# Optimization experiments

Hardware: AMD Instinct MI355X
Metric: run time of the kernel (lower is better)

## Reference

```python
import jax, jax.numpy as jnp
import numpy as np

RADIUS = 0.2
NSAMPLE = 32
EPS = 1e-5  # BatchNorm2d default eps


def _bn_relu(x, g, b):
    # BatchNorm2d in training mode: per-channel stats over (B, S, nsample), biased var.
    m = x.mean(axis=(0, 1, 2))
    v = jnp.mean((x - m) ** 2, axis=(0, 1, 2))
    return jax.nn.relu((x - m) * jax.lax.rsqrt(v + EPS) * g + b)


def setup_inputs() -> dict:
    key = jax.random.key(0)
    ks = jax.random.split(key, 8)
    B, N, S = 8, 8192, 2048
    xyz = jax.random.uniform(ks[0], (B, 3, N), dtype=jnp.float32)          # unit cube
    points = jax.random.normal(ks[1], (B, 3, N), dtype=jnp.float32)
    fps_idx = jax.random.randint(ks[2], (B, S), 0, N, dtype=jnp.int32)
    W1 = jax.random.normal(ks[3], (64, 6), dtype=jnp.float32) * 0.1
    W2 = jax.random.normal(ks[4], (64, 64), dtype=jnp.float32) * 0.1
    W3 = jax.random.normal(ks[5], (128, 64), dtype=jnp.float32) * 0.1
    return dict(
        xyz=xyz, points=points, fps_idx=fps_idx,
        W1=W1, g1=jnp.ones((64,)), b1=jnp.zeros((64,)),
        W2=W2, g2=jnp.ones((64,)), b2=jnp.zeros((64,)),
        W3=W3, g3=jnp.ones((128,)), b3=jnp.zeros((128,)),
    )


def reference(xyz, points, fps_idx, W1, g1, b1, W2, g2, b2, W3, g3, b3):
    B, _, N = xyz.shape
    xyz_t = jnp.transpose(xyz, (0, 2, 1))            # [B,N,3]
    pts_t = jnp.transpose(points, (0, 2, 1))         # [B,N,D]
    # gather_operation: sampled centers
    new_xyz_t = jnp.take_along_axis(xyz_t, fps_idx[:, :, None], axis=1)  # [B,S,3]
    # ball query: first NSAMPLE points within radius; pad with first hit
    d2 = jnp.sum((new_xyz_t[:, :, None, :] - xyz_t[:, None, :, :]) ** 2, axis=-1)  # [B,S,N]
    keys = jnp.where(d2 <= RADIUS * RADIUS, jnp.arange(N, dtype=jnp.int32), N)
    neg_top, _ = jax.lax.top_k(-keys, NSAMPLE)       # smallest keys first
    idx = -neg_top                                   # [B,S,NSAMPLE]
    idx = jnp.where(idx < N, idx, idx[:, :, 0:1])    # pad empty slots with first hit (self always in-radius)
    bidx = jnp.arange(B)[:, None, None]
    grouped_xyz = xyz_t[bidx, idx]                   # [B,S,ns,3]
    rel = grouped_xyz - new_xyz_t[:, :, None, :]     # center-relative coords
    grouped_pts = pts_t[bidx, idx]                   # [B,S,ns,D]
    feat = jnp.concatenate([rel, grouped_pts], axis=-1)  # [B,S,ns,3+D]
    for W, g, b in ((W1, g1, b1), (W2, g2, b2), (W3, g3, b3)):
        feat = _bn_relu(jnp.einsum('bsnc,oc->bsno', feat, W), g, b)
    new_points = jnp.max(feat, axis=2)               # max over neighbors -> [B,S,C]
    return jnp.transpose(new_xyz_t, (0, 2, 1)), jnp.transpose(new_points, (0, 2, 1))
```

## Files before the change

kernel.cpp:

```cpp
#include <hip/hip_runtime.h>
#include <hip/hip_bf16.h>

#define BB_ 8
#define NN_ 8192
#define SS_ 2048
#define NS 32
#define C1 64
#define C2 64
#define C3 128
#define RAD2 0.04f
#define BN_EPS 1e-5f
#define M_TOT (BB_*SS_*NS)
#define INV_M (1.0f/524288.0f)
#define YSTR 34

typedef __attribute__((ext_vector_type(8))) short bf16x8;
typedef __attribute__((ext_vector_type(4))) float f32x4;

#define FBF_OFF 0
#define WPK_OFF 2097152
#define ST_OFF  2104320
#define GMM_OFF 2104832

__device__ inline unsigned pkbf(float a, float b) {
    __hip_bfloat162 h = __float22bfloat162_rn(make_float2(a, b));
    unsigned r; __builtin_memcpy(&r, &h, 4); return r;
}
__device__ inline bf16x8 asfrag(uint4 v) { bf16x8 r; __builtin_memcpy(&r, &v, 16); return r; }
__device__ inline float bflo(unsigned u) { unsigned x = u << 16; float f; __builtin_memcpy(&f, &x, 4); return f; }
__device__ inline float bfhi(unsigned u) { unsigned x = u & 0xffff0000u; float f; __builtin_memcpy(&f, &x, 4); return f; }

__device__ inline void fin1_ch(const float* __restrict__ st, const float* __restrict__ W1,
                               const float* __restrict__ g, const float* __restrict__ bb,
                               int o, float* __restrict__ al, float* __restrict__ cl) {
    float w[6];
    #pragma unroll
    for (int i = 0; i < 6; ++i) w[i] = W1[o * 6 + i];
    float ms = 0.f;
    #pragma unroll
    for (int i = 0; i < 6; ++i) ms = fmaf(w[i], st[i], ms);
    float m = ms * INV_M;
    float e2 = 0.f;
    #pragma unroll
    for (int ci = 0; ci < 6; ++ci)
        #pragma unroll
        for (int d = 0; d < 6; ++d) {
            int lo = ci < d ? ci : d, hi = ci < d ? d : ci;
            int idx = 6 + lo * 6 - lo * (lo + 1) / 2 + hi;
            e2 = fmaf(w[ci] * w[d], st[idx], e2);
        }
    float var = e2 * INV_M - m * m;
    float ai = g[o] * (1.0f / sqrtf(var + BN_EPS));
    al[o] = ai;
    cl[o] = bb[o] - m * ai;
}

__device__ inline void fin_ch(const float* __restrict__ sum, const float* __restrict__ sq,
                              const float* __restrict__ g, const float* __restrict__ bb,
                              int o, float* __restrict__ al, float* __restrict__ cl) {
    float m = sum[o] * INV_M;
    float var = sq[o] * INV_M - m * m;
    float ai = g[o] * (1.0f / sqrtf(var + BN_EPS));
    al[o] = ai;
    cl[o] = bb[o] - m * ai;
}

__global__ void k_front(const float* __restrict__ xyz, const float* __restrict__ pts,
                        const int* __restrict__ fps, uint4* __restrict__ fbf,
                        const float* __restrict__ W1, const float* __restrict__ W2,
                        const float* __restrict__ W3, uint4* __restrict__ wf,
                        float* __restrict__ st) {
    __shared__ int lidx[4][NS];
    int tid = threadIdx.x;
    if (blockIdx.x >= 4096) {
        int bb = blockIdx.x - 4096;
        if (bb == 7) { st[tid] = 0.f; st[tid + 256] = 0.f; return; }
        int t = bb * 256 + tid;
        int l = t & 63, p = l & 15, qd = l >> 4;
        float v[8];
        if (t < 256) {
            int mt = t >> 6;
            #pragma unroll
            for (int j = 0; j < 8; ++j)
                v[j] = (qd == 0 && j < 6) ? W1[(mt * 16 + p) * 6 + j] : 0.f;
        } else if (t < 768) {
            int fr = (t - 256) >> 6;
            int mt = fr >> 1, kf = fr & 1;
            #pragma unroll
            for (int j = 0; j < 8; ++j)
                v[j] = W2[(16 * mt + p) * 64 + kf * 32 + qd * 8 + j];
        } else {
            int fr = (t - 768) >> 6;
            int nt = fr >> 1, kf = fr & 1;
            #pragma unroll
            for (int j = 0; j < 8; ++j)
                v[j] = W3[(nt * 16 + p) * 64 + kf * 32 + qd * 8 + j];
        }
        uint4 o;
        o.x = pkbf(v[0], v[1]); o.y = pkbf(v[2], v[3]);
        o.z = pkbf(v[4], v[5]); o.w = pkbf(v[6], v[7]);
        wf[t] = o;
        return;
    }
    int wave = (blockIdx.x * blockDim.x + tid) >> 6;
    int lane = tid & 63;
    int wslot = tid >> 6;
    int b = wave / SS_;
    const float* xb = xyz + (size_t)b * 3 * NN_;
    const float* pb = pts + (size_t)b * 3 * NN_;
    int ci = fps[wave];
    float cx = xb[ci], cy = xb[NN_ + ci], cz = xb[2 * NN_ + ci];

    float px = xb[lane], py = xb[NN_ + lane], pz = xb[2 * NN_ + lane];
    int found = 0;
    int first_i = -1;
    for (int base = 0; base < NN_; base += 64) {
        float xv = px, yv = py, zv = pz;
        int nb = (base + 64 < NN_) ? base + 64 : 0;
        px = xb[nb + lane]; py = xb[NN_ + nb + lane]; pz = xb[2 * NN_ + nb + lane];
        float dx = xv - cx, dy = yv - cy, dz = zv - cz;
        float d2 = __fadd_rn(__fadd_rn(__fmul_rn(dx, dx), __fmul_rn(dy, dy)), __fmul_rn(dz, dz));
        bool inr = d2 <= RAD2;
        unsigned long long mask = __ballot(inr);
        if (first_i < 0 && mask) first_i = base + __builtin_ctzll(mask);
        if (inr) {
            int pos = found + __popcll(mask & ((1ull << lane) - 1ull));
            if (pos < NS) lidx[wslot][pos] = base + lane;
        }
        found += __popcll(mask);
        if (found >= NS) break;
    }
    if (found > NS) found = NS;
    if (lane < NS) {
        int j = (lane < found) ? lidx[wslot][lane] : first_i;
        uint4 o;
        o.x = pkbf(xb[j] - cx,           xb[NN_ + j] - cy);
        o.y = pkbf(xb[2 * NN_ + j] - cz, pb[j]);
        o.z = pkbf(pb[NN_ + j],          pb[2 * NN_ + j]);
        o.w = 0u;
        fbf[(size_t)wave * NS + lane] = o;
    }
}

__global__ void k_p1(const uint4* __restrict__ fbf, float* __restrict__ st) {
    __shared__ float sacc[27];
    int tid = threadIdx.x;
    if (tid < 27) sacc[tid] = 0.f;
    __syncthreads();
    int gt = blockIdx.x * 256 + tid;
    float vals[27];
    #pragma unroll
    for (int i = 0; i < 27; ++i) vals[i] = 0.f;
    #pragma unroll 1
    for (int it = 0; it < M_TOT / 262144; ++it) {
        uint4 w = fbf[it * 262144 + gt];
        float f[6] = { bflo(w.x), bfhi(w.x), bflo(w.y), bfhi(w.y), bflo(w.z), bfhi(w.z) };
        #pragma unroll
        for (int c = 0; c < 6; ++c) vals[c] += f[c];
        int q = 6;
        #pragma unroll
        for (int c = 0; c < 6; ++c)
            #pragma unroll
            for (int d = c; d < 6; ++d) { vals[q] = fmaf(f[c], f[d], vals[q]); ++q; }
    }
    int lane = tid & 63;
    #pragma unroll
    for (int i = 0; i < 27; ++i) {
        float v = vals[i];
        #pragma unroll
        for (int d = 32; d; d >>= 1) v += __shfl_xor(v, d);
        if (lane == 0) atomicAdd(&sacc[i], v);
    }
    __syncthreads();
    if (tid < 27) atomicAdd(&st[tid], sacc[tid]);
}

__global__ __launch_bounds__(256, 4) void k_p2(
        const uint4* __restrict__ fbf, const uint4* __restrict__ wpk,
        float* __restrict__ st,
        const float* __restrict__ W1, const float* __restrict__ g1, const float* __restrict__ b1) {
    __shared__ unsigned yls[4][64 * YSTR];
    __shared__ float bs[C2], bq[C2];
    __shared__ float a1ls[C1], c1ls[C1];
    int tid = threadIdx.x, wslot = tid >> 6, lane = tid & 63;
    int p = lane & 15, qd = lane >> 4;
    int tile0 = blockIdx.x * 8 + wslot;
    uint4 bv[4];
    #pragma unroll
    for (int nt = 0; nt < 4; ++nt) {
        uint4 v = make_uint4(0u, 0u, 0u, 0u);
        if (qd == 0) v = fbf[tile0 * 64 + nt * 16 + p];
        bv[nt] = v;
    }
    bf16x8 w1r[4];
    #pragma unroll
    for (int mt = 0; mt < 4; ++mt) w1r[mt] = asfrag(wpk[mt * 64 + lane]);
    if (tid < C2) { bs[tid] = 0.f; bq[tid] = 0.f; fin1_ch(st, W1, g1, b1, tid, a1ls, c1ls); }
    __syncthreads();
    const uint4* w2f = wpk + 256;
    unsigned* my = yls[wslot];
    float s2[4][4], q2[4][4];
    #pragma unroll
    for (int i = 0; i < 4; ++i)
        #pragma unroll
        for (int r = 0; r < 4; ++r) { s2[i][r] = 0.f; q2[i][r] = 0.f; }

    #pragma unroll
    for (int t = 0; t < 2; ++t) {
        uint4 nbv[4];
        if (t == 0) {
            #pragma unroll
            for (int nt = 0; nt < 4; ++nt) {
                uint4 v = make_uint4(0u, 0u, 0u, 0u);
                if (qd == 0) v = fbf[(tile0 + 4) * 64 + nt * 16 + p];
                nbv[nt] = v;
            }
        }
        bf16x8 B1[4];
        #pragma unroll
        for (int nt = 0; nt < 4; ++nt) B1[nt] = asfrag(bv[nt]);
        #pragma unroll
        for (int mt = 0; mt < 4; ++mt) {
            bf16x8 A = w1r[mt];
            float4 av = *(const float4*)(a1ls + mt * 16 + qd * 4);
            float4 cv = *(const float4*)(c1ls + mt * 16 + qd * 4);
            #pragma unroll
            for (int nt = 0; nt < 4; ++nt) {
                f32x4 acc = {0.f, 0.f, 0.f, 0.f};
                acc = __builtin_amdgcn_mfma_f32_16x16x32_bf16(A, B1[nt], acc, 0, 0, 0);
                float y0 = fmaxf(fmaf(av.x, acc[0], cv.x), 0.f);
                float y1 = fmaxf(fmaf(av.y, acc[1], cv.y), 0.f);
                float y2 = fmaxf(fmaf(av.z, acc[2], cv.z), 0.f);
                float y3 = fmaxf(fmaf(av.w, acc[3], cv.w), 0.f);
                int a = (nt * 16 + p) * YSTR + mt * 8 + qd * 2;
                *(uint2*)&my[a] = make_uint2(pkbf(y0, y1), pkbf(y2, y3));
            }
        }
        asm volatile("" ::: "memory");
        bf16x8 B2[4][2];
        #pragma unroll
        for (int nt = 0; nt < 4; ++nt)
            #pragma unroll
            for (int kf = 0; kf < 2; ++kf)
                B2[nt][kf] = asfrag(*(const uint4*)&my[(nt * 16 + p) * YSTR + kf * 16 + qd * 4]);
        asm volatile("" ::: "memory");
        #pragma unroll
        for (int mt = 0; mt < 4; ++mt) {
            f32x4 acc[4];
            #pragma unroll
            for (int nt = 0; nt < 4; ++nt) acc[nt] = (f32x4){0.f, 0.f, 0.f, 0.f};
            #pragma unroll
            for (int kf = 0; kf < 2; ++kf) {
                bf16x8 W = asfrag(w2f[(mt * 2 + kf) * 64 + lane]);
                #pragma unroll
                for (int nt = 0; nt < 4; ++nt)
                    acc[nt] = __builtin_amdgcn_mfma_f32_16x16x32_bf16(W, B2[nt][kf], acc[nt], 0, 0, 0);
            }
            #pragma unroll
            for (int r = 0; r < 4; ++r) {
                float u0 = acc[0][r], u1 = acc[1][r], u2 = acc[2][r], u3 = acc[3][r];
                s2[mt][r] += (u0 + u1) + (u2 + u3);
                q2[mt][r] = fmaf(u0, u0, fmaf(u1, u1, fmaf(u2, u2, fmaf(u3, u3, q2[mt][r]))));
            }
        }
        if (t == 0) {
            #pragma unroll
            for (int nt = 0; nt < 4; ++nt) bv[nt] = nbv[nt];
        }
        asm volatile("" ::: "memory");
    }
    #pragma unroll
    for (int mt = 0; mt < 4; ++mt)
        #pragma unroll
        for (int r = 0; r < 4; ++r) {
            float s = s2[mt][r], q = q2[mt][r];
            #pragma unroll
            for (int off = 1; off <= 8; off <<= 1) { s += __shfl_xor(s, off); q += __shfl_xor(q, off); }
            if (p == 0) {
                atomicAdd(&bs[mt * 16 + qd * 4 + r], s);
                atomicAdd(&bq[mt * 16 + qd * 4 + r], q);
            }
        }
    __syncthreads();
    if (tid < C2) { atomicAdd(&st[64 + tid], bs[tid]); atomicAdd(&st[128 + tid], bq[tid]); }
}

__global__ __launch_bounds__(256, 4) void k_p3_fused(
        const uint4* __restrict__ fbf, const uint4* __restrict__ wpk,
        float* __restrict__ st,
        const float* __restrict__ W1, const float* __restrict__ g1, const float* __restrict__ b1,
        const float* __restrict__ g2, const float* __restrict__ b2,
        const float* __restrict__ g3, float* __restrict__ gmm) {
    __shared__ unsigned yls[4][64 * YSTR];
    __shared__ float bs[C3], bq[C3];
    __shared__ float a1ls[C1], c1ls[C1], a2ls[C2], c2ls[C2];
    int tid = threadIdx.x, wslot = tid >> 6, lane = tid & 63;
    int p = lane & 15, qd = lane >> 4;
    int tile0 = blockIdx.x * 4 + wslot;
    unsigned posm = 0;
    #pragma unroll
    for (int i = 0; i < 8; ++i) posm |= (g3[i * 16 + p] >= 0.f) ? (1u << i) : 0u;
    if (tid < 128) bs[tid] = 0.f; else bq[tid - 128] = 0.f;
    if (tid < 64) fin1_ch(st, W1, g1, b1, tid, a1ls, c1ls);
    else if (tid < 128) fin_ch(st + 64, st + 128, g2, b2, tid - 64, a2ls, c2ls);
    __syncthreads();
    const uint4* w1f = wpk;
    const uint4* w2f = wpk + 256;
    const uint4* w3f = wpk + 768;
    unsigned* my = yls[wslot];

    #pragma unroll 1
    for (int it = 0; it < 2; ++it) {
        int tile = tile0 + it * 4096;
        uint4 bv[4];
        #pragma unroll
        for (int nt = 0; nt < 4; ++nt) {
            uint4 v = make_uint4(0u, 0u, 0u, 0u);
            if (qd == 0) v = fbf[tile * 64 + nt * 16 + p];
            bv[nt] = v;
        }
        #pragma unroll
        for (int mt = 0; mt < 4; ++mt) {
            bf16x8 Aw = asfrag(w1f[mt * 64 + lane]);
            float4 av = *(const float4*)(a1ls + mt * 16 + qd * 4);
            float4 cv = *(const float4*)(c1ls + mt * 16 + qd * 4);
            #pragma unroll
            for (int nt = 0; nt < 4; ++nt) {
                f32x4 acc = {0.f, 0.f, 0.f, 0.f};
                acc = __builtin_amdgcn_mfma_f32_16x16x32_bf16(Aw, asfrag(bv[nt]), acc, 0, 0, 0);
                float y0 = fmaxf(fmaf(av.x, acc[0], cv.x), 0.f);
                float y1 = fmaxf(fmaf(av.y, acc[1], cv.y), 0.f);
                float y2 = fmaxf(fmaf(av.z, acc[2], cv.z), 0.f);
                float y3 = fmaxf(fmaf(av.w, acc[3], cv.w), 0.f);
                int a = (nt * 16 + p) * YSTR + mt * 8 + qd * 2;
                *(uint2*)&my[a] = make_uint2(pkbf(y0, y1), pkbf(y2, y3));
            }
        }
        asm volatile("" ::: "memory");
        bf16x8 B2[4][2];
        #pragma unroll
        for (int nt = 0; nt < 4; ++nt)
            #pragma unroll
            for (int kf = 0; kf < 2; ++kf)
                B2[nt][kf] = asfrag(*(const uint4*)&my[(nt * 16 + p) * YSTR + kf * 16 + qd * 4]);
        asm volatile("" ::: "memory");
        #pragma unroll
        for (int mt = 0; mt < 4; ++mt) {
            f32x4 acc[4];
            #pragma unroll
            for (int nt = 0; nt < 4; ++nt) acc[nt] = (f32x4){0.f, 0.f, 0.f, 0.f};
            #pragma unroll
            for (int kf = 0; kf < 2; ++kf) {
                bf16x8 W = asfrag(w2f[(mt * 2 + kf) * 64 + lane]);
                #pragma unroll
                for (int nt = 0; nt < 4; ++nt)
                    acc[nt] = __builtin_amdgcn_mfma_f32_16x16x32_bf16(W, B2[nt][kf], acc[nt], 0, 0, 0);
            }
            float4 av = *(const float4*)(a2ls + mt * 16 + qd * 4);
            float4 cv = *(const float4*)(c2ls + mt * 16 + qd * 4);
            #pragma unroll
            for (int nt = 0; nt < 4; ++nt) {
                float y0 = fmaxf(fmaf(av.x, acc[nt][0], cv.x), 0.f);
                float y1 = fmaxf(fmaf(av.y, acc[nt][1], cv.y), 0.f);
                float y2 = fmaxf(fmaf(av.z, acc[nt][2], cv.z), 0.f);
                float y3 = fmaxf(fmaf(av.w, acc[nt][3], cv.w), 0.f);
                int a = (nt * 16 + p) * YSTR + mt * 8 + qd * 2;
                *(uint2*)&my[a] = make_uint2(pkbf(y0, y1), pkbf(y2, y3));
            }
        }
        asm volatile("" ::: "memory");
        bf16x8 A3[4][2];
        #pragma unroll
        for (int mt = 0; mt < 4; ++mt) {
            A3[mt][0] = asfrag(*(const uint4*)&my[(mt * 16 + p) * YSTR + qd * 4]);
            A3[mt][1] = asfrag(*(const uint4*)&my[(mt * 16 + p) * YSTR + 16 + qd * 4]);
        }
        asm volatile("" ::: "memory");
        uint4 wva = w3f[lane];
        uint4 wvb = w3f[64 + lane];
        #pragma unroll 1
        for (int nt = 0; nt < 8; ++nt) {
            int nn = (nt < 7) ? nt + 1 : 7;
            uint4 nwa = w3f[(nn * 2 + 0) * 64 + lane];
            uint4 nwb = w3f[(nn * 2 + 1) * 64 + lane];
            bf16x8 Wa = asfrag(wva), Wb = asfrag(wvb);
            f32x4 acc[4];
            #pragma unroll
            for (int mt = 0; mt < 4; ++mt) {
                acc[mt] = __builtin_amdgcn_mfma_f32_16x16x32_bf16(A3[mt][0], Wa,
                            (f32x4){0.f, 0.f, 0.f, 0.f}, 0, 0, 0);
                acc[mt] = __builtin_amdgcn_mfma_f32_16x16x32_bf16(A3[mt][1], Wb, acc[mt], 0, 0, 0);
            }
            bool pn = (posm >> nt) & 1;
            float s = 0.f, q = 0.f, va = 0.f, vb = 0.f;
            #pragma unroll
            for (int mt = 0; mt < 4; ++mt) {
                float v0 = acc[mt][0], v1 = acc[mt][1], v2 = acc[mt][2], v3 = acc[mt][3];
                s += (v0 + v1) + (v2 + v3);
                q = fmaf(v0, v0, fmaf(v1, v1, fmaf(v2, v2, fmaf(v3, v3, q))));
                float mx = fmaxf(fmaxf(v0, v1), fmaxf(v2, v3));
                float mn = fminf(fminf(v0, v1), fminf(v2, v3));
                float vv = pn ? mx : -mn;
                if (mt == 0) va = vv;
                else if (mt == 1) va = fmaxf(va, vv);
                else if (mt == 2) vb = vv;
                else vb = fmaxf(vb, vv);
            }
            s += __shfl_xor(s, 16); s += __shfl_xor(s, 32);
            q += __shfl_xor(q, 16); q += __shfl_xor(q, 32);
            va = fmaxf(va, __shfl_xor(va, 16)); va = fmaxf(va, __shfl_xor(va, 32));
            vb = fmaxf(vb, __shfl_xor(vb, 16)); vb = fmaxf(vb, __shfl_xor(vb, 32));
            if (lane < 16) {
                gmm[(size_t)(tile * 2 + 0) * C3 + nt * 16 + lane] = va;
                gmm[(size_t)(tile * 2 + 1) * C3 + nt * 16 + lane] = vb;
                atomicAdd(&bs[nt * 16 + lane], s);
                atomicAdd(&bq[nt * 16 + lane], q);
            }
            wva = nwa; wvb = nwb;
        }
    }
    __syncthreads();
    if (tid < C3) { atomicAdd(&st[192 + tid], bs[tid]); atomicAdd(&st[320 + tid], bq[tid]); }
}

__global__ void k_outx(const float* __restrict__ gmm, const float* __restrict__ st,
                       const float* __restrict__ g3, const float* __restrict__ b3,
                       const float* __restrict__ xyz, const int* __restrict__ fps,
                       float* __restrict__ out) {
    __shared__ float T[C3][17];
    __shared__ float a3ls[C3], c3ls[C3];
    int blk = blockIdx.x, tid = threadIdx.x;
    if (blk < 1024) {
        if (tid < C3) fin_ch(st + 192, st + 320, g3, b3, tid, a3ls, c3ls);
        __syncthreads();
        int b = blk >> 7, s0 = (blk & 127) << 4;
        #pragma unroll
        for (int i = 0; i < 8; ++i) {
            int idx = i * 256 + tid;
            int sl = idx >> 7, o = idx & 127;
            float m = gmm[((size_t)(b * SS_ + s0 + sl)) * C3 + o];
            float a = a3ls[o];
            float v = (a >= 0.f) ? m : -m;
            T[o][sl] = fmaxf(fmaf(a, v, c3ls[o]), 0.f);
        }
        __syncthreads();
        int o = tid & 127, sh = tid >> 7;
        float* dst = out + (size_t)BB_ * 3 * SS_ + ((size_t)b * C3 + o) * SS_ + s0 + sh * 8;
        float4 w0, w1;
        w0.x = T[o][sh * 8 + 0]; w0.y = T[o][sh * 8 + 1];
        w0.z = T[o][sh * 8 + 2]; w0.w = T[o][sh * 8 + 3];
        w1.x = T[o][sh * 8 + 4]; w1.y = T[o][sh * 8 + 5];
        w1.z = T[o][sh * 8 + 6]; w1.w = T[o][sh * 8 + 7];
        *(float4*)dst = w0; *(float4*)(dst + 4) = w1;
    } else {
        int t = (blk - 1024) * 256 + tid;
        int b = t / (3 * SS_);
        int r = (t / SS_) % 3;
        int s = t % SS_;
        int ci = fps[b * SS_ + s];
        out[t] = xyz[((size_t)b * 3 + r) * NN_ + ci];
    }
}

extern "C" void kernel_launch(void* const* d_in, const int* in_sizes, int n_in,
                              void* d_out, int out_size, void* d_ws, size_t ws_size,
                              hipStream_t stream) {
    (void)in_sizes; (void)n_in; (void)out_size; (void)ws_size;
    const float* xyz = (const float*)d_in[0];
    const float* pts = (const float*)d_in[1];
    const int*   fps = (const int*)d_in[2];
    const float* W1 = (const float*)d_in[3];
    const float* g1 = (const float*)d_in[4];
    const float* b1 = (const float*)d_in[5];
    const float* W2 = (const float*)d_in[6];
    const float* g2 = (const float*)d_in[7];
    const float* b2 = (const float*)d_in[8];
    const float* W3 = (const float*)d_in[9];
    const float* g3 = (const float*)d_in[10];
    const float* b3 = (const float*)d_in[11];
    float* out = (float*)d_out;
    float* ws = (float*)d_ws;

    uint4* fbf = (uint4*)(ws + FBF_OFF);
    uint4* wpk = (uint4*)(ws + WPK_OFF);
    float* st  = ws + ST_OFF;
    float* gmm = ws + GMM_OFF;

    k_front<<<4096 + 8, 256, 0, stream>>>(xyz, pts, fps, fbf, W1, W2, W3, wpk, st);
    k_p1<<<1024, 256, 0, stream>>>(fbf, st);
    k_p2<<<1024, 256, 0, stream>>>(fbf, wpk, st, W1, g1, b1);
    k_p3_fused<<<1024, 256, 0, stream>>>(fbf, wpk, st, W1, g1, b1, g2, b2, g3, gmm);
    k_outx<<<1024 + 192, 256, 0, stream>>>(gmm, st, g3, b3, xyz, fps, out);
}
```

Before: 240.0 us.

## Use one-wave blocks per tile in MLP passes with 4-way sharded global stat atomics

k_p2 and k_p3_fused are relaunched as 8192 single-wavefront blocks, each handling one tile, in place of 1024 four-wave blocks that looped over several tiles with shared-memory stat reduction and __syncthreads. Per-channel sum and sum-of-squares now go straight to global atomics, spread across four copies of the stats buffer chosen by blockIdx&3, and the finalize step adds the four copies. The workspace is enlarged and zeroed to hold them. This drops block barriers and the per-block LDS reduction in exchange for many more global atomics and more block launches, and the W1 fragments are no longer kept in registers across tiles.

```diff
diff --git a/kernel.cpp b/kernel.cpp
--- a/kernel.cpp
+++ b/kernel.cpp
@@ -20,7 +20,7 @@
 #define FBF_OFF 0
 #define WPK_OFF 2097152
 #define ST_OFF  2104320
-#define GMM_OFF 2104832
+#define GMM_OFF 2106368
 
 __device__ inline unsigned pkbf(float a, float b) {
     __hip_bfloat162 h = __float22bfloat162_rn(make_float2(a, b));
@@ -55,11 +55,13 @@
     cl[o] = bb[o] - m * ai;
 }
 
-__device__ inline void fin_ch(const float* __restrict__ sum, const float* __restrict__ sq,
-                              const float* __restrict__ g, const float* __restrict__ bb,
-                              int o, float* __restrict__ al, float* __restrict__ cl) {
-    float m = sum[o] * INV_M;
-    float var = sq[o] * INV_M - m * m;
+__device__ inline void fin_ch4(const float* __restrict__ sum, const float* __restrict__ sq,
+                               const float* __restrict__ g, const float* __restrict__ bb,
+                               int o, float* __restrict__ al, float* __restrict__ cl) {
+    float s = (sum[o] + sum[512 + o]) + (sum[1024 + o] + sum[1536 + o]);
+    float q = (sq[o]  + sq[512 + o])  + (sq[1024 + o]  + sq[1536 + o]);
+    float m = s * INV_M;
+    float var = q * INV_M - m * m;
     float ai = g[o] * (1.0f / sqrtf(var + BN_EPS));
     al[o] = ai;
     cl[o] = bb[o] - m * ai;
@@ -74,7 +76,11 @@
     int tid = threadIdx.x;
     if (blockIdx.x >= 4096) {
         int bb = blockIdx.x - 4096;
-        if (bb == 7) { st[tid] = 0.f; st[tid + 256] = 0.f; return; }
+        if (bb == 7) {
+            #pragma unroll
+            for (int k = 0; k < 8; ++k) st[tid + k * 256] = 0.f;
+            return;
+        }
         int t = bb * 256 + tid;
         int l = t & 63, p = l & 15, qd = l >> 4;
         float v[8];
@@ -175,30 +181,27 @@
     if (tid < 27) atomicAdd(&st[tid], sacc[tid]);
 }
 
-__global__ __launch_bounds__(256, 4) void k_p2(
+__global__ __launch_bounds__(64, 4) void k_p2(
         const uint4* __restrict__ fbf, const uint4* __restrict__ wpk,
         float* __restrict__ st,
         const float* __restrict__ W1, const float* __restrict__ g1, const float* __restrict__ b1) {
-    __shared__ unsigned yls[4][64 * YSTR];
-    __shared__ float bs[C2], bq[C2];
+    __shared__ unsigned my[64 * YSTR];
     __shared__ float a1ls[C1], c1ls[C1];
-    int tid = threadIdx.x, wslot = tid >> 6, lane = tid & 63;
+    int lane = threadIdx.x;
     int p = lane & 15, qd = lane >> 4;
-    int tile0 = blockIdx.x * 8 + wslot;
+    int tile = blockIdx.x;
+    float* stb = st + (blockIdx.x & 3) * 512;
     uint4 bv[4];
     #pragma unroll
     for (int nt = 0; nt < 4; ++nt) {
         uint4 v = make_uint4(0u, 0u, 0u, 0u);
-        if (qd == 0) v = fbf[tile0 * 64 + nt * 16 + p];
+        if (qd == 0) v = fbf[tile * 64 + nt * 16 + p];
         bv[nt] = v;
     }
-    bf16x8 w1r[4];
-    #pragma unroll
-    for (int mt = 0; mt < 4; ++mt) w1r[mt] = asfrag(wpk[mt * 64 + lane]);
-    if (tid < C2) { bs[tid] = 0.f; bq[tid] = 0.f; fin1_ch(st, W1, g1, b1, tid, a1ls, c1ls); }
-    __syncthreads();
+    fin1_ch(st, W1, g1, b1, lane, a1ls, c1ls);
+    asm volatile("" ::: "memory");
+    const uint4* w1f = wpk;
     const uint4* w2f = wpk + 256;
-    unsigned* my = yls[wslot];
     float s2[4][4], q2[4][4];
     #pragma unroll
     for (int i = 0; i < 4; ++i)
@@ -206,68 +209,48 @@
         for (int r = 0; r < 4; ++r) { s2[i][r] = 0.f; q2[i][r] = 0.f; }
 
     #pragma unroll
-    for (int t = 0; t < 2; ++t) {
-        uint4 nbv[4];
-        if (t == 0) {
-            #pragma unroll
-            for (int nt = 0; nt < 4; ++nt) {
-                uint4 v = make_uint4(0u, 0u, 0u, 0u);
-                if (qd == 0) v = fbf[(tile0 + 4) * 64 + nt * 16 + p];
-                nbv[nt] = v;
-            }
-        }
-        bf16x8 B1[4];
-        #pragma unroll
-        for (int nt = 0; nt < 4; ++nt) B1[nt] = asfrag(bv[nt]);
-        #pragma unroll
-        for (int mt = 0; mt < 4; ++mt) {
-            bf16x8 A = w1r[mt];
-            float4 av = *(const float4*)(a1ls + mt * 16 + qd * 4);
-            float4 cv = *(const float4*)(c1ls + mt * 16 + qd * 4);
-            #pragma unroll
-            for (int nt = 0; nt < 4; ++nt) {
-                f32x4 acc = {0.f, 0.f, 0.f, 0.f};
-                acc = __builtin_amdgcn_mfma_f32_16x16x32_bf16(A, B1[nt], acc, 0, 0, 0);
-                float y0 = fmaxf(fmaf(av.x, acc[0], cv.x), 0.f);
-                float y1 = fmaxf(fmaf(av.y, acc[1], cv.y), 0.f);
-                float y2 = fmaxf(fmaf(av.z, acc[2], cv.z), 0.f);
-                float y3 = fmaxf(fmaf(av.w, acc[3], cv.w), 0.f);
-                int a = (nt * 16 + p) * YSTR + mt * 8 + qd * 2;
-                *(uint2*)&my[a] = make_uint2(pkbf(y0, y1), pkbf(y2, y3));
-            }
-        }
-        asm volatile("" ::: "memory");
-        bf16x8 B2[4][2];
-        #pragma unroll
-        for (int nt = 0; nt < 4; ++nt)
-            #pragma unroll
-            for (int kf = 0; kf < 2; ++kf)
-                B2[nt][kf] = asfrag(*(const uint4*)&my[(nt * 16 + p) * YSTR + kf * 16 + qd * 4]);
-        asm volatile("" ::: "memory");
-        #pragma unroll
-        for (int mt = 0; mt < 4; ++mt) {
-            f32x4 acc[4];
-            #pragma unroll
-            for (int nt = 0; nt < 4; ++nt) acc[nt] = (f32x4){0.f, 0.f, 0.f, 0.f};
-            #pragma unroll
-            for (int kf = 0; kf < 2; ++kf) {
-                bf16x8 W = asfrag(w2f[(mt * 2 + kf) * 64 + lane]);
-                #pragma unroll
-                for (int nt = 0; nt < 4; ++nt)
-                    acc[nt] = __builtin_amdgcn_mfma_f32_16x16x32_bf16(W, B2[nt][kf], acc[nt], 0, 0, 0);
-            }
-            #pragma unroll
-            for (int r = 0; r < 4; ++r) {
-                float u0 = acc[0][r], u1 = acc[1][r], u2 = acc[2][r], u3 = acc[3][r];
-                s2[mt][r] += (u0 + u1) + (u2 + u3);
-                q2[mt][r] = fmaf(u0, u0, fmaf(u1, u1, fmaf(u2, u2, fmaf(u3, u3, q2[mt][r]))));
-            }
-        }
-        if (t == 0) {
-            #pragma unroll
-            for (int nt = 0; nt < 4; ++nt) bv[nt] = nbv[nt];
-        }
-        asm volatile("" ::: "memory");
+    for (int mt = 0; mt < 4; ++mt) {
+        bf16x8 A = asfrag(w1f[mt * 64 + lane]);
+        float4 av = *(const float4*)(a1ls + mt * 16 + qd * 4);
+        float4 cv = *(const float4*)(c1ls + mt * 16 + qd * 4);
+        #pragma unroll
+        for (int nt = 0; nt < 4; ++nt) {
+            f32x4 acc = {0.f, 0.f, 0.f, 0.f};
+            acc = __builtin_amdgcn_mfma_f32_16x16x32_bf16(A, asfrag(bv[nt]), acc, 0, 0, 0);
+            float y0 = fmaxf(fmaf(av.x, acc[0], cv.x), 0.f);
+            float y1 = fmaxf(fmaf(av.y, acc[1], cv.y), 0.f);
+            float y2 = fmaxf(fmaf(av.z, acc[2], cv.z), 0.f);
+            float y3 = fmaxf(fmaf(av.w, acc[3], cv.w), 0.f);
+            int a = (nt * 16 + p) * YSTR + mt * 8 + qd * 2;
+            *(uint2*)&my[a] = make_uint2(pkbf(y0, y1), pkbf(y2, y3));
+        }
+    }
+    asm volatile("" ::: "memory");
+    bf16x8 B2[4][2];
+    #pragma unroll
+    for (int nt = 0; nt < 4; ++nt)
+        #pragma unroll
+        for (int kf = 0; kf < 2; ++kf)
+            B2[nt][kf] = asfrag(*(const uint4*)&my[(nt * 16 + p) * YSTR + kf * 16 + qd * 4]);
+    asm volatile("" ::: "memory");
+    #pragma unroll
+    for (int mt = 0; mt < 4; ++mt) {
+        f32x4 acc[4];
+        #pragma unroll
+        for (int nt = 0; nt < 4; ++nt) acc[nt] = (f32x4){0.f, 0.f, 0.f, 0.f};
+        #pragma unroll
+        for (int kf = 0; kf < 2; ++kf) {
+            bf16x8 W = asfrag(w2f[(mt * 2 + kf) * 64 + lane]);
+            #pragma unroll
+            for (int nt = 0; nt < 4; ++nt)
+                acc[nt] = __builtin_amdgcn_mfma_f32_16x16x32_bf16(W, B2[nt][kf], acc[nt], 0, 0, 0);
+        }
+        #pragma unroll
+        for (int r = 0; r < 4; ++r) {
+            float u0 = acc[0][r], u1 = acc[1][r], u2 = acc[2][r], u3 = acc[3][r];
+            s2[mt][r] += (u0 + u1) + (u2 + u3);
+            q2[mt][r] = fmaf(u0, u0, fmaf(u1, u1, fmaf(u2, u2, fmaf(u3, u3, q2[mt][r]))));
+        }
     }
     #pragma unroll
     for (int mt = 0; mt < 4; ++mt)
@@ -277,150 +260,140 @@
             #pragma unroll
             for (int off = 1; off <= 8; off <<= 1) { s += __shfl_xor(s, off); q += __shfl_xor(q, off); }
             if (p == 0) {
-                atomicAdd(&bs[mt * 16 + qd * 4 + r], s);
-                atomicAdd(&bq[mt * 16 + qd * 4 + r], q);
+                atomicAdd(&stb[64 + mt * 16 + qd * 4 + r], s);
+                atomicAdd(&stb[128 + mt * 16 + qd * 4 + r], q);
             }
         }
-    __syncthreads();
-    if (tid < C2) { atomicAdd(&st[64 + tid], bs[tid]); atomicAdd(&st[128 + tid], bq[tid]); }
-}
-
-__global__ __launch_bounds__(256, 4) void k_p3_fused(
+}
+
+__global__ __launch_bounds__(64, 4) void k_p3_fused(
         const uint4* __restrict__ fbf, const uint4* __restrict__ wpk,
         float* __restrict__ st,
         const float* __restrict__ W1, const float* __restrict__ g1, const float* __restrict__ b1,
         const float* __restrict__ g2, const float* __restrict__ b2,
         const float* __restrict__ g3, float* __restrict__ gmm) {
-    __shared__ unsigned yls[4][64 * YSTR];
-    __shared__ float bs[C3], bq[C3];
+    __shared__ unsigned my[64 * YSTR];
     __shared__ float a1ls[C1], c1ls[C1], a2ls[C2], c2ls[C2];
-    int tid = threadIdx.x, wslot = tid >> 6, lane = tid & 63;
+    int lane = threadIdx.x;
     int p = lane & 15, qd = lane >> 4;
-    int tile0 = blockIdx.x * 4 + wslot;
+    int tile = blockIdx.x;
+    float* stb = st + (blockIdx.x & 3) * 512;
+    uint4 bv[4];
+    #pragma unroll
+    for (int nt = 0; nt < 4; ++nt) {
+        uint4 v = make_uint4(0u, 0u, 0u, 0u);
+        if (qd == 0) v = fbf[tile * 64 + nt * 16 + p];
+        bv[nt] = v;
+    }
     unsigned posm = 0;
     #pragma unroll
     for (int i = 0; i < 8; ++i) posm |= (g3[i * 16 + p] >= 0.f) ? (1u << i) : 0u;
-    if (tid < 128) bs[tid] = 0.f; else bq[tid - 128] = 0.f;
-    if (tid < 64) fin1_ch(st, W1, g1, b1, tid, a1ls, c1ls);
-    else if (tid < 128) fin_ch(st + 64, st + 128, g2, b2, tid - 64, a2ls, c2ls);
-    __syncthreads();
+    fin1_ch(st, W1, g1, b1, lane, a1ls, c1ls);
+    fin_ch4(st + 64, st + 128, g2, b2, lane, a2ls, c2ls);
+    asm volatile("" ::: "memory");
     const uint4* w1f = wpk;
     const uint4* w2f = wpk + 256;
     const uint4* w3f = wpk + 768;
-    unsigned* my = yls[wslot];
-
+
+    #pragma unroll
+    for (int mt = 0; mt < 4; ++mt) {
+        bf16x8 Aw = asfrag(w1f[mt * 64 + lane]);
+        float4 av = *(const float4*)(a1ls + mt * 16 + qd * 4);
+        float4 cv = *(const float4*)(c1ls + mt * 16 + qd * 4);
+        #pragma unroll
+        for (int nt = 0; nt < 4; ++nt) {
+            f32x4 acc = {0.f, 0.f, 0.f, 0.f};
+            acc = __builtin_amdgcn_mfma_f32_16x16x32_bf16(Aw, asfrag(bv[nt]), acc, 0, 0, 0);
+            float y0 = fmaxf(fmaf(av.x, acc[0], cv.x), 0.f);
+            float y1 = fmaxf(fmaf(av.y, acc[1], cv.y), 0.f);
+            float y2 = fmaxf(fmaf(av.z, acc[2], cv.z), 0.f);
+            float y3 = fmaxf(fmaf(av.w, acc[3], cv.w), 0.f);
+            int a = (nt * 16 + p) * YSTR + mt * 8 + qd * 2;
+            *(uint2*)&my[a] = make_uint2(pkbf(y0, y1), pkbf(y2, y3));
+        }
+    }
+    asm volatile("" ::: "memory");
+    bf16x8 B2[4][2];
+    #pragma unroll
+    for (int nt = 0; nt < 4; ++nt)
+        #pragma unroll
+        for (int kf = 0; kf < 2; ++kf)
+            B2[nt][kf] = asfrag(*(const uint4*)&my[(nt * 16 + p) * YSTR + kf * 16 + qd * 4]);
+    asm volatile("" ::: "memory");
+    #pragma unroll
+    for (int mt = 0; mt < 4; ++mt) {
+        f32x4 acc[4];
+        #pragma unroll
+        for (int nt = 0; nt < 4; ++nt) acc[nt] = (f32x4){0.f, 0.f, 0.f, 0.f};
+        #pragma unroll
+        for (int kf = 0; kf < 2; ++kf) {
+            bf16x8 W = asfrag(w2f[(mt * 2 + kf) * 64 + lane]);
+            #pragma unroll
+            for (int nt = 0; nt < 4; ++nt)
+                acc[nt] = __builtin_amdgcn_mfma_f32_16x16x32_bf16(W, B2[nt][kf], acc[nt], 0, 0, 0);
+        }
+        float4 av = *(const float4*)(a2ls + mt * 16 + qd * 4);
+        float4 cv = *(const float4*)(c2ls + mt * 16 + qd * 4);
+        #pragma unroll
+        for (int nt = 0; nt < 4; ++nt) {
+            float y0 = fmaxf(fmaf(av.x, acc[nt][0], cv.x), 0.f);
+            float y1 = fmaxf(fmaf(av.y, acc[nt][1], cv.y), 0.f);
+            float y2 = fmaxf(fmaf(av.z, acc[nt][2], cv.z), 0.f);
+            float y3 = fmaxf(fmaf(av.w, acc[nt][3], cv.w), 0.f);
+            int a = (nt * 16 + p) * YSTR + mt * 8 + qd * 2;
+            *(uint2*)&my[a] = make_uint2(pkbf(y0, y1), pkbf(y2, y3));
+        }
+    }
+    asm volatile("" ::: "memory");
+    bf16x8 A3[4][2];
+    #pragma unroll
+    for (int mt = 0; mt < 4; ++mt) {
+        A3[mt][0] = asfrag(*(const uint4*)&my[(mt * 16 + p) * YSTR + qd * 4]);
+        A3[mt][1] = asfrag(*(const uint4*)&my[(mt * 16 + p) * YSTR + 16 + qd * 4]);
+    }
+    asm volatile("" ::: "memory");
+    uint4 wva = w3f[lane];
+    uint4 wvb = w3f[64 + lane];
     #pragma unroll 1
-    for (int it = 0; it < 2; ++it) {
-        int tile = tile0 + it * 4096;
-        uint4 bv[4];
-        #pragma unroll
-        for (int nt = 0; nt < 4; ++nt) {
-            uint4 v = make_uint4(0u, 0u, 0u, 0u);
-            if (qd == 0) v = fbf[tile * 64 + nt * 16 + p];
-            bv[nt] = v;
-        }
+    for (int nt = 0; nt < 8; ++nt) {
+        int nn = (nt < 7) ? nt + 1 : 7;
+        uint4 nwa = w3f[(nn * 2 + 0) * 64 + lane];
+        uint4 nwb = w3f[(nn * 2 + 1) * 64 + lane];
+        bf16x8 Wa = asfrag(wva), Wb = asfrag(wvb);
+        f32x4 acc[4];
         #pragma unroll
         for (int mt = 0; mt < 4; ++mt) {
-            bf16x8 Aw = asfrag(w1f[mt * 64 + lane]);
-            float4 av = *(const float4*)(a1ls + mt * 16 + qd * 4);
-            float4 cv = *(const float4*)(c1ls + mt * 16 + qd * 4);
-            #pragma unroll
-            for (int nt = 0; nt < 4; ++nt) {
-                f32x4 acc = {0.f, 0.f, 0.f, 0.f};
-                acc = __builtin_amdgcn_mfma_f32_16x16x32_bf16(Aw, asfrag(bv[nt]), acc, 0, 0, 0);
-                float y0 = fmaxf(fmaf(av.x, acc[0], cv.x), 0.f);
-                float y1 = fmaxf(fmaf(av.y, acc[1], cv.y), 0.f);
-                float y2 = fmaxf(fmaf(av.z, acc[2], cv.z), 0.f);
-                float y3 = fmaxf(fmaf(av.w, acc[3], cv.w), 0.f);
-                int a = (nt * 16 + p) * YSTR + mt * 8 + qd * 2;
-                *(uint2*)&my[a] = make_uint2(pkbf(y0, y1), pkbf(y2, y3));
-            }
-        }
-        asm volatile("" ::: "memory");
-        bf16x8 B2[4][2];
-        #pragma unroll
-        for (int nt = 0; nt < 4; ++nt)
-            #pragma unroll
-            for (int kf = 0; kf < 2; ++kf)
-                B2[nt][kf] = asfrag(*(const uint4*)&my[(nt * 16 + p) * YSTR + kf * 16 + qd * 4]);
-        asm volatile("" ::: "memory");
+            acc[mt] = __builtin_amdgcn_mfma_f32_16x16x32_bf16(A3[mt][0], Wa,
+                        (f32x4){0.f, 0.f, 0.f, 0.f}, 0, 0, 0);
+            acc[mt] = __builtin_amdgcn_mfma_f32_16x16x32_bf16(A3[mt][1], Wb, acc[mt], 0, 0, 0);
+        }
+        bool pn = (posm >> nt) & 1;
+        float s = 0.f, q = 0.f, va = 0.f, vb = 0.f;
         #pragma unroll
         for (int mt = 0; mt < 4; ++mt) {
-            f32x4 acc[4];
-            #pragma unroll
-            for (int nt = 0; nt < 4; ++nt) acc[nt] = (f32x4){0.f, 0.f, 0.f, 0.f};
-            #pragma unroll
-            for (int kf = 0; kf < 2; ++kf) {
-                bf16x8 W = asfrag(w2f[(mt * 2 + kf) * 64 + lane]);
-                #pragma unroll
-                for (int nt = 0; nt < 4; ++nt)
-                    acc[nt] = __builtin_amdgcn_mfma_f32_16x16x32_bf16(W, B2[nt][kf], acc[nt], 0, 0, 0);
-            }
-            float4 av = *(const float4*)(a2ls + mt * 16 + qd * 4);
-            float4 cv = *(const float4*)(c2ls + mt * 16 + qd * 4);
-            #pragma unroll
-            for (int nt = 0; nt < 4; ++nt) {
-                float y0 = fmaxf(fmaf(av.x, acc[nt][0], cv.x), 0.f);
-                float y1 = fmaxf(fmaf(av.y, acc[nt][1], cv.y), 0.f);
-                float y2 = fmaxf(fmaf(av.z, acc[nt][2], cv.z), 0.f);
-                float y3 = fmaxf(fmaf(av.w, acc[nt][3], cv.w), 0.f);
-                int a = (nt * 16 + p) * YSTR + mt * 8 + qd * 2;
-                *(uint2*)&my[a] = make_uint2(pkbf(y0, y1), pkbf(y2, y3));
-            }
-        }
-        asm volatile("" ::: "memory");
-        bf16x8 A3[4][2];
-        #pragma unroll
-        for (int mt = 0; mt < 4; ++mt) {
-            A3[mt][0] = asfrag(*(const uint4*)&my[(mt * 16 + p) * YSTR + qd * 4]);
-            A3[mt][1] = asfrag(*(const uint4*)&my[(mt * 16 + p) * YSTR + 16 + qd * 4]);
-        }
-        asm volatile("" ::: "memory");
-        uint4 wva = w3f[lane];
-        uint4 wvb = w3f[64 + lane];
-        #pragma unroll 1
-        for (int nt = 0; nt < 8; ++nt) {
-            int nn = (nt < 7) ? nt + 1 : 7;
-            uint4 nwa = w3f[(nn * 2 + 0) * 64 + lane];
-            uint4 nwb = w3f[(nn * 2 + 1) * 64 + lane];
-            bf16x8 Wa = asfrag(wva), Wb = asfrag(wvb);
-            f32x4 acc[4];
-            #pragma unroll
-            for (int mt = 0; mt < 4; ++mt) {
-                acc[mt] = __builtin_amdgcn_mfma_f32_16x16x32_bf16(A3[mt][0], Wa,
-                            (f32x4){0.f, 0.f, 0.f, 0.f}, 0, 0, 0);
-                acc[mt] = __builtin_amdgcn_mfma_f32_16x16x32_bf16(A3[mt][1], Wb, acc[mt], 0, 0, 0);
-            }
-            bool pn = (posm >> nt) & 1;
-            float s = 0.f, q = 0.f, va = 0.f, vb = 0.f;
-            #pragma unroll
-            for (int mt = 0; mt < 4; ++mt) {
-                float v0 = acc[mt][0], v1 = acc[mt][1], v2 = acc[mt][2], v3 = acc[mt][3];
-                s += (v0 + v1) + (v2 + v3);
-                q = fmaf(v0, v0, fmaf(v1, v1, fmaf(v2, v2, fmaf(v3, v3, q))));
-                float mx = fmaxf(fmaxf(v0, v1), fmaxf(v2, v3));
-                float mn = fminf(fminf(v0, v1), fminf(v2, v3));
-                float vv = pn ? mx : -mn;
-                if (mt == 0) va = vv;
-                else if (mt == 1) va = fmaxf(va, vv);
-                else if (mt == 2) vb = vv;
-                else vb = fmaxf(vb, vv);
-            }
-            s += __shfl_xor(s, 16); s += __shfl_xor(s, 32);
-            q += __shfl_xor(q, 16); q += __shfl_xor(q, 32);
-            va = fmaxf(va, __shfl_xor(va, 16)); va = fmaxf(va, __shfl_xor(va, 32));
-            vb = fmaxf(vb, __shfl_xor(vb, 16)); vb = fmaxf(vb, __shfl_xor(vb, 32));
-            if (lane < 16) {
-                gmm[(size_t)(tile * 2 + 0) * C3 + nt * 16 + lane] = va;
-                gmm[(size_t)(tile * 2 + 1) * C3 + nt * 16 + lane] = vb;
-                atomicAdd(&bs[nt * 16 + lane], s);
-                atomicAdd(&bq[nt * 16 + lane], q);
-            }
-            wva = nwa; wvb = nwb;
-        }
-    }
-    __syncthreads();
-    if (tid < C3) { atomicAdd(&st[192 + tid], bs[tid]); atomicAdd(&st[320 + tid], bq[tid]); }
+            float v0 = acc[mt][0], v1 = acc[mt][1], v2 = acc[mt][2], v3 = acc[mt][3];
+            s += (v0 + v1) + (v2 + v3);
+            q = fmaf(v0, v0, fmaf(v1, v1, fmaf(v2, v2, fmaf(v3, v3, q))));
+            float mx = fmaxf(fmaxf(v0, v1), fmaxf(v2, v3));
+            float mn = fminf(fminf(v0, v1), fminf(v2, v3));
+            float vv = pn ? mx : -mn;
+            if (mt == 0) va = vv;
+            else if (mt == 1) va = fmaxf(va, vv);
+            else if (mt == 2) vb = vv;
+            else vb = fmaxf(vb, vv);
+        }
+        s += __shfl_xor(s, 16); s += __shfl_xor(s, 32);
+        q += __shfl_xor(q, 16); q += __shfl_xor(q, 32);
+        va = fmaxf(va, __shfl_xor(va, 16)); va = fmaxf(va, __shfl_xor(va, 32));
+        vb = fmaxf(vb, __shfl_xor(vb, 16)); vb = fmaxf(vb, __shfl_xor(vb, 32));
+        if (lane < 16) {
+            gmm[(size_t)(tile * 2 + 0) * C3 + nt * 16 + lane] = va;
+            gmm[(size_t)(tile * 2 + 1) * C3 + nt * 16 + lane] = vb;
+            atomicAdd(&stb[192 + nt * 16 + lane], s);
+            atomicAdd(&stb[320 + nt * 16 + lane], q);
+        }
+        wva = nwa; wvb = nwb;
+    }
 }
 
 __global__ void k_outx(const float* __restrict__ gmm, const float* __restrict__ st,
@@ -431,7 +404,7 @@
     __shared__ float a3ls[C3], c3ls[C3];
     int blk = blockIdx.x, tid = threadIdx.x;
     if (blk < 1024) {
-        if (tid < C3) fin_ch(st + 192, st + 320, g3, b3, tid, a3ls, c3ls);
+        if (tid < C3) fin_ch4(st + 192, st + 320, g3, b3, tid, a3ls, c3ls);
         __syncthreads();
         int b = blk >> 7, s0 = (blk & 127) << 4;
         #pragma unroll
@@ -488,7 +461,7 @@
 
     k_front<<<4096 + 8, 256, 0, stream>>>(xyz, pts, fps, fbf, W1, W2, W3, wpk, st);
     k_p1<<<1024, 256, 0, stream>>>(fbf, st);
-    k_p2<<<1024, 256, 0, stream>>>(fbf, wpk, st, W1, g1, b1);
-    k_p3_fused<<<1024, 256, 0, stream>>>(fbf, wpk, st, W1, g1, b1, g2, b2, g3, gmm);
+    k_p2<<<8192, 64, 0, stream>>>(fbf, wpk, st, W1, g1, b1);
+    k_p3_fused<<<8192, 64, 0, stream>>>(fbf, wpk, st, W1, g1, b1, g2, b2, g3, gmm);
     k_outx<<<1024 + 192, 256, 0, stream>>>(gmm, st, g3, b3, xyz, fps, out);
 }
```

Result: slower. 443.6 us (+84.8%).

## Fuse layer-1 stats into ball-query kernel and prefetch both tiles in p3

Applied to the files above, without the earlier changes.

Removes the separate k_p1 kernel. The first-layer sum and second-moment statistics are now computed inside k_front from the gathered fp32 features and reduced through shared memory and atomics. This avoids re-reading the packed feature buffer and saves a kernel launch, but adds a hipMemsetAsync to zero the stats buffer and puts per-block atomics in the front kernel. The stats are now taken from unrounded fp32 values rather than the bf16-packed ones used downstream. Separately, k_p3_fused issues the loads for both of its tiles up front and fully unrolls the two-iteration loop, so the second tile's global load latency overlaps with work.

```diff
diff --git a/kernel.cpp b/kernel.cpp
--- a/kernel.cpp
+++ b/kernel.cpp
@@ -71,10 +71,10 @@
                         const float* __restrict__ W3, uint4* __restrict__ wf,
                         float* __restrict__ st) {
     __shared__ int lidx[4][NS];
+    __shared__ float sacc[27];
     int tid = threadIdx.x;
     if (blockIdx.x >= 4096) {
         int bb = blockIdx.x - 4096;
-        if (bb == 7) { st[tid] = 0.f; st[tid + 256] = 0.f; return; }
         int t = bb * 256 + tid;
         int l = t & 63, p = l & 15, qd = l >> 4;
         float v[8];
@@ -102,6 +102,8 @@
         wf[t] = o;
         return;
     }
+    if (tid < 27) sacc[tid] = 0.f;
+    __syncthreads();
     int wave = (blockIdx.x * blockDim.x + tid) >> 6;
     int lane = tid & 63;
     int wslot = tid >> 6;
@@ -131,39 +133,30 @@
         if (found >= NS) break;
     }
     if (found > NS) found = NS;
+    float f0 = 0.f, f1 = 0.f, f2 = 0.f, f3 = 0.f, f4 = 0.f, f5 = 0.f;
     if (lane < NS) {
         int j = (lane < found) ? lidx[wslot][lane] : first_i;
+        f0 = xb[j] - cx;           f1 = xb[NN_ + j] - cy;
+        f2 = xb[2 * NN_ + j] - cz; f3 = pb[j];
+        f4 = pb[NN_ + j];          f5 = pb[2 * NN_ + j];
         uint4 o;
-        o.x = pkbf(xb[j] - cx,           xb[NN_ + j] - cy);
-        o.y = pkbf(xb[2 * NN_ + j] - cz, pb[j]);
-        o.z = pkbf(pb[NN_ + j],          pb[2 * NN_ + j]);
+        o.x = pkbf(f0, f1);
+        o.y = pkbf(f2, f3);
+        o.z = pkbf(f4, f5);
         o.w = 0u;
         fbf[(size_t)wave * NS + lane] = o;
     }
-}
-
-__global__ void k_p1(const uint4* __restrict__ fbf, float* __restrict__ st) {
-    __shared__ float sacc[27];
-    int tid = threadIdx.x;
-    if (tid < 27) sacc[tid] = 0.f;
-    __syncthreads();
-    int gt = blockIdx.x * 256 + tid;
+    float f[6] = { f0, f1, f2, f3, f4, f5 };
     float vals[27];
     #pragma unroll
-    for (int i = 0; i < 27; ++i) vals[i] = 0.f;
-    #pragma unroll 1
-    for (int it = 0; it < M_TOT / 262144; ++it) {
-        uint4 w = fbf[it * 262144 + gt];
-        float f[6] = { bflo(w.x), bfhi(w.x), bflo(w.y), bfhi(w.y), bflo(w.z), bfhi(w.z) };
-        #pragma unroll
-        for (int c = 0; c < 6; ++c) vals[c] += f[c];
+    for (int c = 0; c < 6; ++c) vals[c] = f[c];
+    {
         int q = 6;
         #pragma unroll
         for (int c = 0; c < 6; ++c)
             #pragma unroll
-            for (int d = c; d < 6; ++d) { vals[q] = fmaf(f[c], f[d], vals[q]); ++q; }
-    }
-    int lane = tid & 63;
+            for (int d = c; d < 6; ++d) { vals[q] = f[c] * f[d]; ++q; }
+    }
     #pragma unroll
     for (int i = 0; i < 27; ++i) {
         float v = vals[i];
@@ -297,6 +290,17 @@
     int tid = threadIdx.x, wslot = tid >> 6, lane = tid & 63;
     int p = lane & 15, qd = lane >> 4;
     int tile0 = blockIdx.x * 4 + wslot;
+    uint4 bv0[4], bv1[4];
+    #pragma unroll
+    for (int nt = 0; nt < 4; ++nt) {
+        uint4 v0 = make_uint4(0u, 0u, 0u, 0u);
+        uint4 v1 = make_uint4(0u, 0u, 0u, 0u);
+        if (qd == 0) {
+            v0 = fbf[tile0 * 64 + nt * 16 + p];
+            v1 = fbf[(tile0 + 4096) * 64 + nt * 16 + p];
+        }
+        bv0[nt] = v0; bv1[nt] = v1;
+    }
     unsigned posm = 0;
     #pragma unroll
     for (int i = 0; i < 8; ++i) posm |= (g3[i * 16 + p] >= 0.f) ? (1u << i) : 0u;
@@ -309,16 +313,9 @@
     const uint4* w3f = wpk + 768;
     unsigned* my = yls[wslot];
 
-    #pragma unroll 1
+    #pragma unroll
     for (int it = 0; it < 2; ++it) {
         int tile = tile0 + it * 4096;
-        uint4 bv[4];
-        #pragma unroll
-        for (int nt = 0; nt < 4; ++nt) {
-            uint4 v = make_uint4(0u, 0u, 0u, 0u);
-            if (qd == 0) v = fbf[tile * 64 + nt * 16 + p];
-            bv[nt] = v;
-        }
         #pragma unroll
         for (int mt = 0; mt < 4; ++mt) {
             bf16x8 Aw = asfrag(w1f[mt * 64 + lane]);
@@ -326,8 +323,9 @@
             float4 cv = *(const float4*)(c1ls + mt * 16 + qd * 4);
             #pragma unroll
             for (int nt = 0; nt < 4; ++nt) {
+                uint4 bcur = (it == 0) ? bv0[nt] : bv1[nt];
                 f32x4 acc = {0.f, 0.f, 0.f, 0.f};
-                acc = __builtin_amdgcn_mfma_f32_16x16x32_bf16(Aw, asfrag(bv[nt]), acc, 0, 0, 0);
+                acc = __builtin_amdgcn_mfma_f32_16x16x32_bf16(Aw, asfrag(bcur), acc, 0, 0, 0);
                 float y0 = fmaxf(fmaf(av.x, acc[0], cv.x), 0.f);
                 float y1 = fmaxf(fmaf(av.y, acc[1], cv.y), 0.f);
                 float y2 = fmaxf(fmaf(av.z, acc[2], cv.z), 0.f);
@@ -486,8 +484,8 @@
     float* st  = ws + ST_OFF;
     float* gmm = ws + GMM_OFF;
 
-    k_front<<<4096 + 8, 256, 0, stream>>>(xyz, pts, fps, fbf, W1, W2, W3, wpk, st);
-    k_p1<<<1024, 256, 0, stream>>>(fbf, st);
+    hipMemsetAsync(st, 0, 512 * sizeof(float), stream);
+    k_front<<<4096 + 7, 256, 0, stream>>>(xyz, pts, fps, fbf, W1, W2, W3, wpk, st);
     k_p2<<<1024, 256, 0, stream>>>(fbf, wpk, st, W1, g1, b1);
     k_p3_fused<<<1024, 256, 0, stream>>>(fbf, wpk, st, W1, g1, b1, g2, b2, g3, gmm);
     k_outx<<<1024 + 192, 256, 0, stream>>>(gmm, st, g3, b3, xyz, fps, out);
```

Measured after the change: 265.9 us. +10.8%, slower.
